# Optimization experiments

Hardware: AMD Instinct MI355X
Metric: run time of the kernel (lower is better)

Reference implementation:

```python
import jax, jax.numpy as jnp
import numpy as np

ALPHA = 0.25
GAMMA = 2.0
VAR0, VAR1 = 0.1, 0.2  # torch.Tensor([0.1, 0.2]) variances in encode
EPS = 1e-4


def _center_size(boxes):
    # corner (x1,y1,x2,y2) -> center (cx,cy,w,h)
    return jnp.concatenate([(boxes[:, :2] + boxes[:, 2:]) * 0.5,
                            boxes[:, 2:] - boxes[:, :2]], axis=1)


def _jaccard(a, b):
    # a: [A,4] anchors, b: [T,4] targets, corner form -> IoU [A,T]
    lt = jnp.maximum(a[:, None, :2], b[None, :, :2])
    rb = jnp.minimum(a[:, None, 2:], b[None, :, 2:])
    wh = jnp.clip(rb - lt, 0.0)
    inter = wh[..., 0] * wh[..., 1]
    area_a = (a[:, 2] - a[:, 0]) * (a[:, 3] - a[:, 1])
    area_b = (b[:, 2] - b[:, 0]) * (b[:, 3] - b[:, 1])
    return inter / (area_a[:, None] + area_b[None, :] - inter)


def _encode(matched, priors_cf):
    # matched: corner form [P,4]; priors_cf: center form [P,4]
    g_cxcy = ((matched[:, :2] + matched[:, 2:]) * 0.5 - priors_cf[:, :2]) / (VAR0 * priors_cf[:, 2:])
    g_wh = jnp.log((matched[:, 2:] - matched[:, :2]) / priors_cf[:, 2:]) / VAR1
    return jnp.concatenate([g_cxcy, g_wh], axis=1)


def _per_image(cla, reg, target, anchor, anchor_cf):
    # cla [A,C], reg [A,4], target [T,5]
    valid = target[:, 4] != -1.0                      # padded targets (label -1) are excluded
    has_valid = jnp.any(valid)
    cla = jnp.clip(cla, EPS, 1.0 - EPS)
    iou = _jaccard(anchor, target[:, :4])             # [A,T]
    iou = jnp.where(valid[None, :], iou, -1.0)        # mask padded targets (valid IoUs are >= 0)
    iou_argmax = jnp.argmax(iou, axis=1)              # [A]
    iou_max = jnp.take_along_axis(iou, iou_argmax[:, None], axis=1)[:, 0]
    pos = iou_max >= 0.5
    num_pos = jnp.sum(pos)
    assigned = target[iou_argmax]                     # [A,5] gather of matched gt

    C = cla.shape[1]
    onehot = jax.nn.one_hot(assigned[:, 4].astype(jnp.int32), C, dtype=cla.dtype)
    labels = jnp.full_like(cla, -1.0)
    labels = jnp.where(iou_max[:, None] < 0.4, 0.0, labels)
    labels = jnp.where(pos[:, None], onehot, labels)

    is_one = labels == 1.0
    alpha_factor = jnp.where(is_one, ALPHA, 1.0 - ALPHA)
    focal_weight = alpha_factor * jnp.where(is_one, 1.0 - cla, cla) ** GAMMA
    bce = -(labels * jnp.log(cla) + (1.0 - labels) * jnp.log1p(-cla))
    cls_loss = jnp.where(labels != -1.0, focal_weight * bce, 0.0)
    cls_loss = cls_loss.sum() / jnp.maximum(num_pos.astype(cla.dtype), 1.0)

    # smooth-L1 on positive anchors only; original takes .mean() over [P,4]
    enc_gt = _encode(assigned[:, :4], anchor_cf)      # [A,4]
    diff = jnp.abs(enc_gt - reg)
    sl1 = jnp.where(diff <= 1.0 / 9.0, 0.5 * 9.0 * diff * diff, diff - 0.5 / 9.0)
    denom = jnp.maximum(num_pos * 4, 1).astype(cla.dtype)
    reg_loss = jnp.where(num_pos > 0, jnp.sum(sl1 * pos[:, None]) / denom, 0.0)

    cls_loss = jnp.where(has_valid, cls_loss, 0.0)
    reg_loss = jnp.where(has_valid, reg_loss, 0.0)
    return cls_loss, reg_loss


def setup_inputs() -> dict:
    key = jax.random.key(0)
    ks = jax.random.split(key, 7)
    B, A, C, T = 8, 100000, 80, 50
    clas = jax.random.uniform(ks[0], (B, A, C), jnp.float32, 0.01, 0.99)
    regs = jax.random.normal(ks[1], (B, A, 4), jnp.float32)
    # anchors: valid corner boxes inside a ~1024x1024 image
    axy = jax.random.uniform(ks[2], (1, A, 2), jnp.float32, 0.0, 900.0)
    awh = jax.random.uniform(ks[3], (1, A, 2), jnp.float32, 16.0, 120.0)
    anchors = jnp.concatenate([axy, axy + awh], axis=-1)
    # targets: valid gt boxes with class id in [0, C) stored as float in column 4
    txy = jax.random.uniform(ks[4], (B, T, 2), jnp.float32, 0.0, 800.0)
    twh = jax.random.uniform(ks[5], (B, T, 2), jnp.float32, 20.0, 220.0)
    lab = jax.random.randint(ks[6], (B, T, 1), 0, C).astype(jnp.float32)
    targets = jnp.concatenate([txy, txy + twh, lab], axis=-1)
    return {"clas": clas, "regs": regs, "anchors": anchors, "targets": targets}


def reference(clas, regs, anchors, targets):
    anchor = anchors[0]                               # [A,4]
    anchor_cf = _center_size(anchor)
    cls_l, reg_l = jax.vmap(_per_image, in_axes=(0, 0, 0, None, None))(
        clas, regs, targets, anchor, anchor_cf)
    return (jnp.mean(cls_l, keepdims=True), jnp.mean(reg_l, keepdims=True))
```

## Files before the change

kernel.cpp:

```cpp
#include <hip/hip_runtime.h>

#define A_COUNT 100000
#define B_COUNT 8
#define C_COUNT 80
#define T_COUNT 50
#define BLOCK   256

__global__ __launch_bounds__(BLOCK) void retina_main(
    const float* __restrict__ clas,
    const float* __restrict__ regs,
    const float* __restrict__ anchors,
    const float* __restrict__ targets,
    float* __restrict__ ws_cls,
    float* __restrict__ ws_reg,
    int*   __restrict__ ws_pos)
{
    __shared__ float s_tgt[T_COUNT * 5];
    __shared__ int   s_state[BLOCK];
    __shared__ float s_c[4], s_r[4];
    __shared__ int   s_p[4];

    const int b    = blockIdx.y;
    const int base = blockIdx.x * BLOCK;
    const int tid  = threadIdx.x;

    for (int i = tid; i < T_COUNT * 5; i += BLOCK)
        s_tgt[i] = targets[b * T_COUNT * 5 + i];
    __syncthreads();

    const int a = base + tid;
    int   state  = -1;
    float my_reg = 0.0f;
    bool  my_pos = false;

    if (a < A_COUNT) {
        const float4 an = ((const float4*)anchors)[a];
        const float area_a = (an.z - an.x) * (an.w - an.y);

        float best = -1.0f;
        int   bestIdx = 0;
        bool  anyValid = false;

        #pragma unroll 1
        for (int t = 0; t < T_COUNT; ++t) {
            const float tx1 = s_tgt[t * 5 + 0];
            const float ty1 = s_tgt[t * 5 + 1];
            const float tx2 = s_tgt[t * 5 + 2];
            const float ty2 = s_tgt[t * 5 + 3];
            const float lab = s_tgt[t * 5 + 4];
            float iou = -1.0f;
            if (lab != -1.0f) {
                anyValid = true;
                const float lx = fmaxf(an.x, tx1), ly = fmaxf(an.y, ty1);
                const float rx = fminf(an.z, tx2), ry = fminf(an.w, ty2);
                const float w = fmaxf(rx - lx, 0.0f);
                const float h = fmaxf(ry - ly, 0.0f);
                const float inter  = w * h;
                const float area_b = (tx2 - tx1) * (ty2 - ty1);
                iou = inter / (area_a + area_b - inter);
            }
            if (iou > best) { best = iou; bestIdx = t; }
        }

        if (anyValid) {
            if (best >= 0.5f) {
                state  = (int)s_tgt[bestIdx * 5 + 4];
                my_pos = true;
                const float4 rg = ((const float4*)regs)[(size_t)b * A_COUNT + a];
                const float tx1 = s_tgt[bestIdx * 5 + 0];
                const float ty1 = s_tgt[bestIdx * 5 + 1];
                const float tx2 = s_tgt[bestIdx * 5 + 2];
                const float ty2 = s_tgt[bestIdx * 5 + 3];
                const float pcx = (an.x + an.z) * 0.5f, pcy = (an.y + an.w) * 0.5f;
                const float pw  = an.z - an.x,          ph  = an.w - an.y;
                const float mcx = (tx1 + tx2) * 0.5f,   mcy = (ty1 + ty2) * 0.5f;
                const float mw  = tx2 - tx1,            mh  = ty2 - ty1;
                const float e0 = (mcx - pcx) / (0.1f * pw);
                const float e1 = (mcy - pcy) / (0.1f * ph);
                const float e2 = __logf(mw / pw) * 5.0f;
                const float e3 = __logf(mh / ph) * 5.0f;
                const float d0 = fabsf(e0 - rg.x);
                const float d1 = fabsf(e1 - rg.y);
                const float d2 = fabsf(e2 - rg.z);
                const float d3 = fabsf(e3 - rg.w);
                const float th = 1.0f / 9.0f;
                const float c59 = 0.5f / 9.0f;
                const float s0 = (d0 <= th) ? 4.5f * d0 * d0 : d0 - c59;
                const float s1 = (d1 <= th) ? 4.5f * d1 * d1 : d1 - c59;
                const float s2 = (d2 <= th) ? 4.5f * d2 * d2 : d2 - c59;
                const float s3 = (d3 <= th) ? 4.5f * d3 * d3 : d3 - c59;
                my_reg = s0 + s1 + s2 + s3;
            } else if (best < 0.4f) {
                state = 128;
            }
        }
    }
    s_state[tid] = state;
    __syncthreads();

    const int nA     = min(BLOCK, A_COUNT - base);
    const int count4 = nA * (C_COUNT / 4);
    const float4* cl4 = (const float4*)(clas + ((size_t)b * A_COUNT + base) * C_COUNT);

    float cls_local = 0.0f;
    for (int i = tid; i < count4; i += BLOCK) {
        const int a_local = i / (C_COUNT / 4);
        const int c0      = (i % (C_COUNT / 4)) * 4;
        const int st      = s_state[a_local];
        if (st == -1) continue;
        const float4 v = cl4[i];
        const float pv[4] = { v.x, v.y, v.z, v.w };
        #pragma unroll
        for (int j = 0; j < 4; ++j) {
            const float p  = fminf(fmaxf(pv[j], 1e-4f), 1.0f - 1e-4f);
            const bool one = (c0 + j) == st;
            const float q  = one ? p : (1.0f - p);
            const float af = one ? 0.25f : 0.75f;
            const float om = 1.0f - q;
            cls_local += af * om * om * (-__logf(q));
        }
    }

    float r0 = cls_local, r1 = my_reg;
    const unsigned long long bal = __ballot(my_pos);
    const int posc = __popcll(bal);
    #pragma unroll
    for (int off = 32; off > 0; off >>= 1) {
        r0 += __shfl_down(r0, off);
        r1 += __shfl_down(r1, off);
    }
    const int wave = tid >> 6, lane = tid & 63;
    if (lane == 0) { s_c[wave] = r0; s_r[wave] = r1; s_p[wave] = posc; }
    __syncthreads();
    if (tid == 0) {
        float tc = 0.0f, tr = 0.0f; int tp = 0;
        #pragma unroll
        for (int w = 0; w < 4; ++w) { tc += s_c[w]; tr += s_r[w]; tp += s_p[w]; }
        atomicAdd(&ws_cls[b], tc);
        atomicAdd(&ws_reg[b], tr);
        atomicAdd(&ws_pos[b], tp);
    }
}

__global__ void retina_final(const float* __restrict__ ws_cls,
                             const float* __restrict__ ws_reg,
                             const int*   __restrict__ ws_pos,
                             float* __restrict__ out)
{
    const int tid = threadIdx.x;
    float cl = 0.0f, rl = 0.0f;
    if (tid < B_COUNT) {
        const int   npi = ws_pos[tid];
        const float np  = (float)npi;
        cl = ws_cls[tid] / fmaxf(np, 1.0f);
        rl = (npi > 0) ? ws_reg[tid] / (np * 4.0f) : 0.0f;
    }
    #pragma unroll
    for (int off = 4; off > 0; off >>= 1) {
        cl += __shfl_down(cl, off);
        rl += __shfl_down(rl, off);
    }
    if (tid == 0) {
        out[0] = cl * (1.0f / (float)B_COUNT);
        out[1] = rl * (1.0f / (float)B_COUNT);
    }
}

extern "C" void kernel_launch(void* const* d_in, const int* in_sizes, int n_in,
                              void* d_out, int out_size, void* d_ws, size_t ws_size,
                              hipStream_t stream) {
    const float* clas    = (const float*)d_in[0];
    const float* regs    = (const float*)d_in[1];
    const float* anchors = (const float*)d_in[2];
    const float* targets = (const float*)d_in[3];

    float* ws_cls = (float*)d_ws;
    float* ws_reg = ws_cls + B_COUNT;
    int*   ws_pos = (int*)(ws_reg + B_COUNT);

    hipMemsetAsync(d_ws, 0, (2 * B_COUNT) * sizeof(float) + B_COUNT * sizeof(int), stream);

    dim3 grid((A_COUNT + BLOCK - 1) / BLOCK, B_COUNT);
    retina_main<<<grid, BLOCK, 0, stream>>>(clas, regs, anchors, targets,
                                            ws_cls, ws_reg, ws_pos);
    retina_final<<<1, 64, 0, stream>>>(ws_cls, ws_reg, ws_pos, (float*)d_out);
}
```

Measured before the change: 401.7 us.

## Unroll class loss loop with nontemporal loads and per-positive correction

The class-loss loop now treats every element as a negative, computing 0.75*p^2*(-log(1-p)) for each. It then applies a per-positive-anchor correction that reloads the one matched probability and swaps in the positive term. Full blocks use a fixed five-by-four unrolled schedule of nontemporal float4 loads with incremental anchor/class index tracking instead of a division per element. Ignored anchors are masked with a zero weight, so their loads are still issued rather than skipped. This is meant to cut index arithmetic and per-element branching and to let more loads be in flight, at the cost of loading data for ignored anchors.

```diff
diff --git a/kernel.cpp b/kernel.cpp
--- a/kernel.cpp
+++ b/kernel.cpp
@@ -5,6 +5,10 @@
 #define C_COUNT 80
 #define T_COUNT 50
 #define BLOCK   256
+#define NF4     (C_COUNT / 4)
+#define FULL4   (BLOCK * NF4)
+
+typedef float f4v __attribute__((ext_vector_type(4)));
 
 __global__ __launch_bounds__(BLOCK) void retina_main(
     const float* __restrict__ clas,
@@ -98,27 +102,54 @@
     s_state[tid] = state;
     __syncthreads();
 
-    const int nA     = min(BLOCK, A_COUNT - base);
-    const int count4 = nA * (C_COUNT / 4);
-    const float4* cl4 = (const float4*)(clas + ((size_t)b * A_COUNT + base) * C_COUNT);
-
+    const int nA = min(BLOCK, A_COUNT - base);
+    const f4v* cl4 = (const f4v*)(clas + ((size_t)b * A_COUNT + base) * C_COUNT);
     float cls_local = 0.0f;
-    for (int i = tid; i < count4; i += BLOCK) {
-        const int a_local = i / (C_COUNT / 4);
-        const int c0      = (i % (C_COUNT / 4)) * 4;
-        const int st      = s_state[a_local];
-        if (st == -1) continue;
-        const float4 v = cl4[i];
-        const float pv[4] = { v.x, v.y, v.z, v.w };
+
+    if (nA == BLOCK) {
+        int aL = tid / NF4;
+        int cL = tid - aL * NF4;
         #pragma unroll
-        for (int j = 0; j < 4; ++j) {
-            const float p  = fminf(fmaxf(pv[j], 1e-4f), 1.0f - 1e-4f);
-            const bool one = (c0 + j) == st;
-            const float q  = one ? p : (1.0f - p);
-            const float af = one ? 0.25f : 0.75f;
-            const float om = 1.0f - q;
-            cls_local += af * om * om * (-__logf(q));
-        }
+        for (int ko = 0; ko < 5; ++ko) {
+            f4v v[4];
+            #pragma unroll
+            for (int u = 0; u < 4; ++u)
+                v[u] = __builtin_nontemporal_load(&cl4[tid + (ko * 4 + u) * BLOCK]);
+            #pragma unroll
+            for (int u = 0; u < 4; ++u) {
+                const int st  = s_state[aL];
+                const float w = (st == -1) ? 0.0f : 0.75f;
+                #pragma unroll
+                for (int j = 0; j < 4; ++j) {
+                    float p = fminf(fmaxf(v[u][j], 1e-4f), 1.0f - 1e-4f);
+                    float l = __logf(1.0f - p);
+                    cls_local = fmaf(p * p * l, -w, cls_local);
+                }
+                aL += 12; cL += 16;
+                if (cL >= NF4) { cL -= NF4; ++aL; }
+            }
+        }
+    } else {
+        const int count4 = nA * NF4;
+        for (int i = tid; i < count4; i += BLOCK) {
+            const int st = s_state[i / NF4];
+            if (st == -1) continue;
+            const f4v v = __builtin_nontemporal_load(&cl4[i]);
+            #pragma unroll
+            for (int j = 0; j < 4; ++j) {
+                float p = fminf(fmaxf(v[j], 1e-4f), 1.0f - 1e-4f);
+                float l = __logf(1.0f - p);
+                cls_local = fmaf(p * p * l, -0.75f, cls_local);
+            }
+        }
+    }
+
+    if (my_pos) {
+        float p = clas[((size_t)b * A_COUNT + a) * C_COUNT + state];
+        p = fminf(fmaxf(p, 1e-4f), 1.0f - 1e-4f);
+        const float om = 1.0f - p;
+        cls_local += 0.25f * om * om * (-__logf(p))
+                   - 0.75f * p * p * (-__logf(om));
     }
 
     float r0 = cls_local, r1 = my_reg;
```

New measurement: 401.5 us. No clear change (-0.1%).

## Split focal loss into per-anchor weight pass and uniform streaming reduction

Applied to the files above, without the earlier changes.

Rewrites the classification loss algebraically: every non-ignored anchor gets a uniform negative-term weight, and the single positive class is handled by a per-anchor correction computed in the IoU kernel. This lets the large class-probability tensor be read by a separate, branch-free streaming kernel that issues several independent float4 loads per thread, with no per-element state lookup. The cost is a second launch plus a per-anchor weight buffer written and then read back. Ignored anchors are now read anyway with zero weight, so they no longer skip memory traffic.

```diff
diff --git a/kernel.cpp b/kernel.cpp
--- a/kernel.cpp
+++ b/kernel.cpp
@@ -5,18 +5,25 @@
 #define C_COUNT 80
 #define T_COUNT 50
 #define BLOCK   256
-
-__global__ __launch_bounds__(BLOCK) void retina_main(
+#define NF4     (C_COUNT / 4)
+#define IMG_F4  (A_COUNT * NF4)
+#define GX_B    1024
+#define TPI     (GX_B * BLOCK)
+#define KB_IT   8
+
+typedef float f4v __attribute__((ext_vector_type(4)));
+
+__global__ __launch_bounds__(BLOCK) void retina_state(
     const float* __restrict__ clas,
     const float* __restrict__ regs,
     const float* __restrict__ anchors,
     const float* __restrict__ targets,
     float* __restrict__ ws_cls,
     float* __restrict__ ws_reg,
-    int*   __restrict__ ws_pos)
+    int*   __restrict__ ws_pos,
+    float* __restrict__ ws_w)
 {
     __shared__ float s_tgt[T_COUNT * 5];
-    __shared__ int   s_state[BLOCK];
     __shared__ float s_c[4], s_r[4];
     __shared__ int   s_p[4];
 
@@ -29,8 +36,8 @@
     __syncthreads();
 
     const int a = base + tid;
-    int   state  = -1;
     float my_reg = 0.0f;
+    float my_fix = 0.0f;
     bool  my_pos = false;
 
     if (a < A_COUNT) {
@@ -62,10 +69,19 @@
             if (iou > best) { best = iou; bestIdx = t; }
         }
 
+        float wgt = 0.0f;
         if (anyValid) {
             if (best >= 0.5f) {
-                state  = (int)s_tgt[bestIdx * 5 + 4];
+                wgt    = 0.75f;
                 my_pos = true;
+                const int cls_id = (int)s_tgt[bestIdx * 5 + 4];
+
+                float p = clas[((size_t)b * A_COUNT + a) * C_COUNT + cls_id];
+                p = fminf(fmaxf(p, 1e-4f), 1.0f - 1e-4f);
+                const float om = 1.0f - p;
+                my_fix = 0.25f * om * om * (-__logf(p))
+                       - 0.75f * p * p   * (-__logf(om));
+
                 const float4 rg = ((const float4*)regs)[(size_t)b * A_COUNT + a];
                 const float tx1 = s_tgt[bestIdx * 5 + 0];
                 const float ty1 = s_tgt[bestIdx * 5 + 1];
@@ -83,7 +99,7 @@
                 const float d1 = fabsf(e1 - rg.y);
                 const float d2 = fabsf(e2 - rg.z);
                 const float d3 = fabsf(e3 - rg.w);
-                const float th = 1.0f / 9.0f;
+                const float th  = 1.0f / 9.0f;
                 const float c59 = 0.5f / 9.0f;
                 const float s0 = (d0 <= th) ? 4.5f * d0 * d0 : d0 - c59;
                 const float s1 = (d1 <= th) ? 4.5f * d1 * d1 : d1 - c59;
@@ -91,37 +107,13 @@
                 const float s3 = (d3 <= th) ? 4.5f * d3 * d3 : d3 - c59;
                 my_reg = s0 + s1 + s2 + s3;
             } else if (best < 0.4f) {
-                state = 128;
+                wgt = 0.75f;
             }
         }
-    }
-    s_state[tid] = state;
-    __syncthreads();
-
-    const int nA     = min(BLOCK, A_COUNT - base);
-    const int count4 = nA * (C_COUNT / 4);
-    const float4* cl4 = (const float4*)(clas + ((size_t)b * A_COUNT + base) * C_COUNT);
-
-    float cls_local = 0.0f;
-    for (int i = tid; i < count4; i += BLOCK) {
-        const int a_local = i / (C_COUNT / 4);
-        const int c0      = (i % (C_COUNT / 4)) * 4;
-        const int st      = s_state[a_local];
-        if (st == -1) continue;
-        const float4 v = cl4[i];
-        const float pv[4] = { v.x, v.y, v.z, v.w };
-        #pragma unroll
-        for (int j = 0; j < 4; ++j) {
-            const float p  = fminf(fmaxf(pv[j], 1e-4f), 1.0f - 1e-4f);
-            const bool one = (c0 + j) == st;
-            const float q  = one ? p : (1.0f - p);
-            const float af = one ? 0.25f : 0.75f;
-            const float om = 1.0f - q;
-            cls_local += af * om * om * (-__logf(q));
-        }
-    }
-
-    float r0 = cls_local, r1 = my_reg;
+        ws_w[b * A_COUNT + a] = wgt;
+    }
+
+    float r0 = my_fix, r1 = my_reg;
     const unsigned long long bal = __ballot(my_pos);
     const int posc = __popcll(bal);
     #pragma unroll
@@ -136,9 +128,58 @@
         float tc = 0.0f, tr = 0.0f; int tp = 0;
         #pragma unroll
         for (int w = 0; w < 4; ++w) { tc += s_c[w]; tr += s_r[w]; tp += s_p[w]; }
+        if (tc != 0.0f) atomicAdd(&ws_cls[b], tc);
+        if (tr != 0.0f) atomicAdd(&ws_reg[b], tr);
+        if (tp != 0)    atomicAdd(&ws_pos[b], tp);
+    }
+}
+
+__global__ __launch_bounds__(BLOCK) void retina_focal(
+    const float* __restrict__ clas,
+    const float* __restrict__ ws_w,
+    float* __restrict__ ws_cls)
+{
+    __shared__ float s_c[4];
+
+    const int b   = blockIdx.y;
+    const int tid = threadIdx.x;
+    const int i0  = blockIdx.x * BLOCK + tid;
+
+    const f4v*   cl4 = (const f4v*)(clas + (size_t)b * A_COUNT * C_COUNT);
+    const float* wgt = ws_w + b * A_COUNT;
+
+    f4v  v[KB_IT];
+    bool ok[KB_IT];
+    #pragma unroll
+    for (int k = 0; k < KB_IT; ++k) {
+        const int i = i0 + k * TPI;
+        ok[k] = (i < IMG_F4);
+        if (ok[k]) v[k] = cl4[i];
+    }
+
+    float acc = 0.0f;
+    #pragma unroll
+    for (int k = 0; k < KB_IT; ++k) {
+        if (!ok[k]) continue;
+        const int i = i0 + k * TPI;
+        const float w = wgt[i / 20];
+        #pragma unroll
+        for (int j = 0; j < 4; ++j) {
+            float p = fminf(fmaxf(v[k][j], 1e-4f), 1.0f - 1e-4f);
+            float l = __logf(1.0f - p);
+            acc = fmaf(p * p * l, -w, acc);
+        }
+    }
+
+    #pragma unroll
+    for (int off = 32; off > 0; off >>= 1)
+        acc += __shfl_down(acc, off);
+    const int wave = tid >> 6, lane = tid & 63;
+    if (lane == 0) s_c[wave] = acc;
+    __syncthreads();
+    if (tid == 0) {
+        float tc = s_c[0] + s_c[1] + s_c[2] + s_c[3];
         atomicAdd(&ws_cls[b], tc);
-        atomicAdd(&ws_reg[b], tr);
-        atomicAdd(&ws_pos[b], tp);
     }
 }
 
@@ -177,11 +218,16 @@
     float* ws_cls = (float*)d_ws;
     float* ws_reg = ws_cls + B_COUNT;
     int*   ws_pos = (int*)(ws_reg + B_COUNT);
-
-    hipMemsetAsync(d_ws, 0, (2 * B_COUNT) * sizeof(float) + B_COUNT * sizeof(int), stream);
-
-    dim3 grid((A_COUNT + BLOCK - 1) / BLOCK, B_COUNT);
-    retina_main<<<grid, BLOCK, 0, stream>>>(clas, regs, anchors, targets,
-                                            ws_cls, ws_reg, ws_pos);
+    float* ws_w   = (float*)d_ws + 32;
+
+    hipMemsetAsync(d_ws, 0, 32 * sizeof(float), stream);
+
+    dim3 gridA((A_COUNT + BLOCK - 1) / BLOCK, B_COUNT);
+    retina_state<<<gridA, BLOCK, 0, stream>>>(clas, regs, anchors, targets,
+                                              ws_cls, ws_reg, ws_pos, ws_w);
+
+    dim3 gridB(GX_B, B_COUNT);
+    retina_focal<<<gridB, BLOCK, 0, stream>>>(clas, ws_w, ws_cls);
+
     retina_final<<<1, 64, 0, stream>>>(ws_cls, ws_reg, ws_pos, (float*)d_out);
 }
```

Result: slower. 479.6 us (+19.4%).
